# Kernel optimization log

Measured on AMD Instinct MI355X. Metric: run time of the kernel, lower is better.

Reference implementation:

```python
import jax, jax.numpy as jnp
import numpy as np

NUM_USERS = 100000
NUM_ITEMS = 200000
EMB_DIM = 64
NUM_LAYERS = 3
NUM_INTER = 1000000
BATCH = 16384


def setup_inputs() -> dict:
    key = jax.random.key(0)
    k1, k2, k3, k4, k5, k6, k7 = jax.random.split(key, 7)
    # xavier-uniform-ish init for embeddings
    bound_u = float(np.sqrt(6.0 / (NUM_USERS + EMB_DIM)))
    bound_i = float(np.sqrt(6.0 / (NUM_ITEMS + EMB_DIM)))
    user_emb = jax.random.uniform(k1, (NUM_USERS, EMB_DIM), jnp.float32, -bound_u, bound_u)
    item_emb = jax.random.uniform(k2, (NUM_ITEMS, EMB_DIM), jnp.float32, -bound_i, bound_i)
    layer_weights = jax.random.uniform(k3, (NUM_LAYERS + 1,), jnp.float32)
    inter_users = jax.random.randint(k4, (NUM_INTER,), 0, NUM_USERS, jnp.int32)
    inter_items = jax.random.randint(k5, (NUM_INTER,), 0, NUM_ITEMS, jnp.int32)
    user_ids = jax.random.randint(k6, (BATCH,), 0, NUM_USERS, jnp.int32)
    item_ids = jax.random.randint(k7, (BATCH,), 0, NUM_ITEMS, jnp.int32)
    return {
        "user_emb": user_emb,
        "item_emb": item_emb,
        "layer_weights": layer_weights,
        "inter_users": inter_users,
        "inter_items": inter_items,
        "user_ids": user_ids,
        "item_ids": item_ids,
    }


def reference(user_emb, item_emb, layer_weights, inter_users, inter_items, user_ids, item_ids):
    n_users = user_emb.shape[0]
    n_items = item_emb.shape[0]
    n_nodes = n_users + n_items

    # Symmetrized bipartite edge list: (u -> i+n_users) and (i+n_users -> u)
    rows = inter_users
    cols = inter_items + n_users
    src = jnp.concatenate([rows, cols])  # [2E]
    dst = jnp.concatenate([cols, rows])  # [2E]

    # Symmetric degree normalization: D^{-1/2} A D^{-1/2}
    deg = jax.ops.segment_sum(jnp.ones_like(src, dtype=jnp.float32), src,
                              num_segments=n_nodes)
    dinv = jnp.where(deg > 0, jax.lax.rsqrt(jnp.maximum(deg, 1.0)) * (deg > 0), 0.0)
    dinv = jnp.where(deg > 0, deg ** -0.5, 0.0)
    edge_w = dinv[src] * dinv[dst]  # [2E]

    emb = jnp.concatenate([user_emb, item_emb], axis=0)  # [N, D]
    weights = jax.nn.softmax(layer_weights)

    final = weights[0] * emb
    for layer in range(NUM_LAYERS):
        # SpMM: out[src] += w * emb[dst]
        emb = jax.ops.segment_sum(edge_w[:, None] * emb[dst], src,
                                  num_segments=n_nodes)
        final = final + weights[layer + 1] * emb

    u_final = final[:n_users]
    i_final = final[n_users:]

    user_vectors = u_final[user_ids]   # [B, D]
    item_vectors = i_final[item_ids]   # [B, D]
    scores = jnp.sum(user_vectors * item_vectors, axis=1)  # [B]
    return scores
```

## Files before the change

kernel.cpp:

```cpp
#include <hip/hip_runtime.h>
#include <math.h>

#define NUM_USERS 100000
#define NUM_ITEMS 200000
#define N_NODES   300000
#define EMB       64
#define NUM_INTER 1000000
#define N_EDGES   (2 * NUM_INTER)
#define MAX_SLOTS (N_EDGES + 3 * N_NODES + 16)
#define BATCH     16384

#define BSHIFT 9
#define BNODES 512
#define NBKT   ((N_NODES + BNODES - 1) / BNODES)
#define CAP    6144
#define EDGES_PER_BLOCK 4096
#define AB_BLOCKS ((NUM_INTER + EDGES_PER_BLOCK - 1) / EDGES_PER_BLOCK)

#define CONV_BLOCKS ((N_NODES * 8 + 255) / 256)
#define MARK_BLOCKS ((BATCH * 2) / 256)
#define PROP_BLOCKS ((N_NODES * 8 + 255) / 256)

typedef float    vfloat4 __attribute__((ext_vector_type(4)));
typedef int      vint4   __attribute__((ext_vector_type(4)));
typedef _Float16 half8   __attribute__((ext_vector_type(8)));

__global__ __launch_bounds__(256) void bucket_scatter_k(
        const int* __restrict__ iu, const int* __restrict__ ii,
        int* __restrict__ cursor , uint2* __restrict__ pairs) {
    __shared__ int hist[NBKT];
    __shared__ int gbase[NBKT];
    int tid = threadIdx.x;
    for (int b = tid; b < NBKT; b += 256) hist[b] = 0;
    __syncthreads();

    int e0 = blockIdx.x * EDGES_PER_BLOCK;
    int u[16], it[16];
    unsigned pk[32];
    #pragma unroll
    for (int k = 0; k < 16; ++k) {
        int e = e0 + k * 256 + tid;
        bool v = (e < NUM_INTER);
        u[k]  = v ? iu[e] : -1;
        it[k] = v ? (NUM_USERS + ii[e]) : -1;
    }
    #pragma unroll
    for (int k = 0; k < 16; ++k) {
        if (u[k] >= 0) {
            int b0 = u[k] >> BSHIFT;
            int r0 = atomicAdd(&hist[b0], 1);
            pk[2 * k] = ((unsigned)b0 << 13) | (unsigned)r0;
            int b1 = it[k] >> BSHIFT;
            int r1 = atomicAdd(&hist[b1], 1);
            pk[2 * k + 1] = ((unsigned)b1 << 13) | (unsigned)r1;
        }
    }
    __syncthreads();
    for (int b = tid; b < NBKT; b += 256) {
        int c = hist[b];
        if (c) gbase[b] = atomicAdd(&cursor[b * 16], c);
    }
    __syncthreads();
    #pragma unroll
    for (int k = 0; k < 16; ++k) {
        if (u[k] >= 0) {
            unsigned p0 = pk[2 * k];
            int b0 = (int)(p0 >> 13);
            int s0 = gbase[b0] + (int)(p0 & 0x1fffu);
            if (s0 < CAP) pairs[(size_t)b0 * CAP + s0] = make_uint2((unsigned)u[k], (unsigned)it[k]);
            unsigned p1 = pk[2 * k + 1];
            int b1 = (int)(p1 >> 13);
            int s1 = gbase[b1] + (int)(p1 & 0x1fffu);
            if (s1 < CAP) pairs[(size_t)b1 * CAP + s1] = make_uint2((unsigned)it[k], (unsigned)u[k]);
        }
    }
}

__global__ __launch_bounds__(256) void bucket_deg_k(
        const int* __restrict__ cursor, const uint2* __restrict__ pairs,
        int* __restrict__ deg, float* __restrict__ dinv, float* __restrict__ d2,
        float* __restrict__ rcp, int* __restrict__ lofs, int* __restrict__ bkt_padded) {
    __shared__ int cnt[BNODES];
    __shared__ int sc[256];
    int b = blockIdx.x, tid = threadIdx.x;
    cnt[tid] = 0; cnt[tid + 256] = 0;
    __syncthreads();
    int n = cursor[b * 16]; if (n > CAP) n = CAP;
    const uint2* p = pairs + (size_t)b * CAP;
    for (int j = tid; j < n; j += 256)
        atomicAdd(&cnt[p[j].x & (BNODES - 1)], 1);
    __syncthreads();

    int l0 = 2 * tid, l1 = 2 * tid + 1;
    int c0 = cnt[l0], c1 = cnt[l1];
    int p0 = (c0 + 3) & ~3, p1 = (c1 + 3) & ~3;
    int s = p0 + p1;
    sc[tid] = s;
    __syncthreads();
    for (int o = 1; o < 256; o <<= 1) {
        int x = (tid >= o) ? sc[tid - o] : 0;
        __syncthreads();
        sc[tid] += x;
        __syncthreads();
    }
    int excl = sc[tid] - s;
    int g0 = (b << BSHIFT) + l0;
    int g1 = g0 + 1;
    if (g0 < N_NODES) {
        deg[g0] = c0;
        float fd = (float)c0;
        dinv[g0] = (c0 > 0) ? (1.0f / sqrtf(fd)) : 0.0f;
        d2[g0]   = (c0 > 0) ? (1.0f / fd) : 0.0f;
        rcp[g0]  = (c0 > 0) ? sqrtf(fd) : 0.0f;
        lofs[g0] = excl;
    }
    if (g1 < N_NODES) {
        deg[g1] = c1;
        float fd = (float)c1;
        dinv[g1] = (c1 > 0) ? (1.0f / sqrtf(fd)) : 0.0f;
        d2[g1]   = (c1 > 0) ? (1.0f / fd) : 0.0f;
        rcp[g1]  = (c1 > 0) ? sqrtf(fd) : 0.0f;
        lofs[g1] = excl + p0;
    }
    if (tid == 255) bkt_padded[b] = sc[255];
}

__global__ void csr_mid_k(const int* __restrict__ bkt_padded, int* __restrict__ bkt_base,
                          int* __restrict__ row_start,
                          const float* __restrict__ lw, float* __restrict__ w,
                          _Float16* __restrict__ semb, _Float16* __restrict__ z1,
                          _Float16* __restrict__ z2) {
    __shared__ int lds[1024];
    int t = threadIdx.x;
    int v = (t < NBKT) ? bkt_padded[t] : 0;
    lds[t] = v;
    __syncthreads();
    for (int o = 1; o < 1024; o <<= 1) {
        int x = (t >= o) ? lds[t - o] : 0;
        __syncthreads();
        lds[t] += x;
        __syncthreads();
    }
    if (t < NBKT) bkt_base[t] = lds[t] - v;
    if (t == 1023) row_start[N_NODES] = lds[1023];
    if (t < 96) {
        unsigned* p = (t < 32) ? (unsigned*)semb : (t < 64) ? (unsigned*)z1 : (unsigned*)z2;
        p[(size_t)N_NODES * 32 + (t & 31)] = 0u;
    }
    if (t == 0) {
        float a = lw[0], b = lw[1], c = lw[2], d = lw[3];
        float m = fmaxf(fmaxf(a, b), fmaxf(c, d));
        float e0 = expf(a - m), e1 = expf(b - m), e2 = expf(c - m), e3 = expf(d - m);
        float sm = e0 + e1 + e2 + e3;
        w[0] = e0 / sm; w[1] = e1 / sm; w[2] = e2 / sm; w[3] = e3 / sm;
    }
}

__global__ __launch_bounds__(256) void bucket_build_k(
        const int* __restrict__ cursor, const uint2* __restrict__ pairs,
        const int* __restrict__ bkt_base, const int* __restrict__ lofs,
        int* __restrict__ row_start, int* __restrict__ nbr,
        const float* __restrict__ dinv,
        const float* __restrict__ ue, const float* __restrict__ ie,
        _Float16* __restrict__ semb) {
    int bid = blockIdx.x;
    int tid = threadIdx.x;
    if (bid >= NBKT) {
        int t = (bid - NBKT) * 256 + tid;
        int node = t >> 3;
        int q = t & 7;
        if (node >= N_NODES) return;
        const float4* src = (node < NUM_USERS)
            ? (const float4*)ue + (size_t)node * 16
            : (const float4*)ie + (size_t)(node - NUM_USERS) * 16;
        float4 f0 = src[q * 2];
        float4 f1 = src[q * 2 + 1];
        float s = dinv[node];
        half8 h;
        h[0] = (_Float16)(s * f0.x); h[1] = (_Float16)(s * f0.y);
        h[2] = (_Float16)(s * f0.z); h[3] = (_Float16)(s * f0.w);
        h[4] = (_Float16)(s * f1.x); h[5] = (_Float16)(s * f1.y);
        h[6] = (_Float16)(s * f1.z); h[7] = (_Float16)(s * f1.w);
        ((half8*)semb)[(size_t)node * 8 + q] = h;
        return;
    }
    __shared__ int ofs[BNODES];
    __shared__ int cnt2[BNODES];
    int b = bid;
    int base = bkt_base[b];
    {
        int g0 = (b << BSHIFT) + tid;
        int g1 = g0 + 256;
        int o0 = (g0 < N_NODES) ? lofs[g0] : 0;
        int o1 = (g1 < N_NODES) ? lofs[g1] : 0;
        ofs[tid] = o0; ofs[tid + 256] = o1;
        cnt2[tid] = 0; cnt2[tid + 256] = 0;
        if (g0 < N_NODES) row_start[g0] = base + o0;
        if (g1 < N_NODES) row_start[g1] = base + o1;
    }
    __syncthreads();
    int n = cursor[b * 16]; if (n > CAP) n = CAP;
    const uint2* p = pairs + (size_t)b * CAP;
    for (int j = tid; j < n; j += 256) {
        uint2 pr = p[j];
        int l = (int)(pr.x & (BNODES - 1));
        int r = atomicAdd(&cnt2[l], 1);
        nbr[base + ofs[l] + r] = (int)pr.y;
    }
}

__global__ void mark_prop_k(const int* __restrict__ row_start, const int* __restrict__ nbr,
                            const int* __restrict__ deg, const float* __restrict__ d2,
                            const _Float16* __restrict__ semb, _Float16* __restrict__ z1,
                            const int* __restrict__ uid, const int* __restrict__ iid,
                            int* __restrict__ flag) {
    int bid = blockIdx.x;
    if (bid < MARK_BLOCKS) {
        int t = bid * 256 + threadIdx.x;
        int slot = t >> 1;
        int node = (t & 1) ? (NUM_USERS + iid[slot]) : uid[slot];
        flag[node] = 1;
        int beg = row_start[node];
        int lim = beg + deg[node];
        for (int j = beg; j < lim; ++j) flag[nbr[j]] = 1;
        return;
    }
    int t = (bid - MARK_BLOCKS) * 256 + threadIdx.x;
    int node = t >> 3;
    int q = t & 7;
    if (node >= N_NODES) return;
    int beg = row_start[node], end = row_start[node + 1];
    int lim = beg + deg[node];
    const half8* src = (const half8*)semb;
    float a0 = 0.f, a1 = 0.f, a2 = 0.f, a3 = 0.f, a4 = 0.f, a5 = 0.f, a6 = 0.f, a7 = 0.f;
    for (int j = beg; j < end; j += 8) {
        vint4 na = __builtin_nontemporal_load((const vint4*)(nbr + j));
        vint4 nb = __builtin_nontemporal_load((const vint4*)(nbr + j + 4));
        #pragma unroll
        for (int k = 0; k < 8; ++k) {
            int id = (j + k < lim) ? ((k < 4) ? na[k] : nb[k - 4]) : N_NODES;
            half8 h = src[(size_t)id * 8 + q];
            a0 += (float)h[0]; a1 += (float)h[1]; a2 += (float)h[2]; a3 += (float)h[3];
            a4 += (float)h[4]; a5 += (float)h[5]; a6 += (float)h[6]; a7 += (float)h[7];
        }
    }
    float s = d2[node];
    half8 r;
    r[0] = (_Float16)(s * a0); r[1] = (_Float16)(s * a1);
    r[2] = (_Float16)(s * a2); r[3] = (_Float16)(s * a3);
    r[4] = (_Float16)(s * a4); r[5] = (_Float16)(s * a5);
    r[6] = (_Float16)(s * a6); r[7] = (_Float16)(s * a7);
    __builtin_nontemporal_store(r, (half8*)z1 + (size_t)node * 8 + q);
}

__global__ void prop_masked_k(const int* __restrict__ row_start, const int* __restrict__ nbr,
                              const int* __restrict__ deg, const float* __restrict__ d2,
                              const int* __restrict__ flag,
                              const _Float16* __restrict__ in, _Float16* __restrict__ out) {
    int t = blockIdx.x * blockDim.x + threadIdx.x;
    int node = t >> 3;
    int q = t & 7;
    if (node >= N_NODES) return;
    if (!flag[node]) return;
    int beg = row_start[node], end = row_start[node + 1];
    int lim = beg + deg[node];
    const half8* src = (const half8*)in;
    float a0 = 0.f, a1 = 0.f, a2 = 0.f, a3 = 0.f, a4 = 0.f, a5 = 0.f, a6 = 0.f, a7 = 0.f;
    for (int j = beg; j < end; j += 8) {
        vint4 na = __builtin_nontemporal_load((const vint4*)(nbr + j));
        vint4 nb = __builtin_nontemporal_load((const vint4*)(nbr + j + 4));
        #pragma unroll
        for (int k = 0; k < 8; ++k) {
            int id = (j + k < lim) ? ((k < 4) ? na[k] : nb[k - 4]) : N_NODES;
            half8 h = src[(size_t)id * 8 + q];
            a0 += (float)h[0]; a1 += (float)h[1]; a2 += (float)h[2]; a3 += (float)h[3];
            a4 += (float)h[4]; a5 += (float)h[5]; a6 += (float)h[6]; a7 += (float)h[7];
        }
    }
    float s = d2[node];
    half8 r;
    r[0] = (_Float16)(s * a0); r[1] = (_Float16)(s * a1);
    r[2] = (_Float16)(s * a2); r[3] = (_Float16)(s * a3);
    r[4] = (_Float16)(s * a4); r[5] = (_Float16)(s * a5);
    r[6] = (_Float16)(s * a6); r[7] = (_Float16)(s * a7);
    __builtin_nontemporal_store(r, (half8*)out + (size_t)node * 8 + q);
}

__global__ void fused_score_k(const int* __restrict__ row_start, const int* __restrict__ nbr,
                              const int* __restrict__ deg,
                              const float* __restrict__ dinv, const float* __restrict__ rcp,
                              const float* __restrict__ ue, const float* __restrict__ ie,
                              const _Float16* __restrict__ z1, const _Float16* __restrict__ z2,
                              const int* __restrict__ uid, const int* __restrict__ iid,
                              const float* __restrict__ w4, float* __restrict__ out) {
    int t = blockIdx.x * blockDim.x + threadIdx.x;
    int slot = t >> 4;
    if (slot >= BATCH) return;
    int within = t & 15;
    int side = within >> 3;
    int q = within & 7;

    int node;
    const float4* erow;
    if (side == 0) {
        int u = uid[slot];
        node = u;
        erow = (const float4*)ue + (size_t)u * 16;
    } else {
        int ii_ = iid[slot];
        node = NUM_USERS + ii_;
        erow = (const float4*)ie + (size_t)ii_ * 16;
    }

    float w0 = w4[0], w1 = w4[1], w2 = w4[2], w3 = w4[3];
    int beg = row_start[node], end = row_start[node + 1];
    int lim = beg + deg[node];
    const half8* z2v = (const half8*)z2;

    float a0 = 0.f, a1 = 0.f, a2 = 0.f, a3 = 0.f, a4 = 0.f, a5 = 0.f, a6 = 0.f, a7 = 0.f;
    for (int j = beg; j < end; j += 8) {
        vint4 na = __builtin_nontemporal_load((const vint4*)(nbr + j));
        vint4 nb = __builtin_nontemporal_load((const vint4*)(nbr + j + 4));
        #pragma unroll
        for (int k = 0; k < 8; ++k) {
            int id = (j + k < lim) ? ((k < 4) ? na[k] : nb[k - 4]) : N_NODES;
            half8 h = z2v[(size_t)id * 8 + q];
            a0 += (float)h[0]; a1 += (float)h[1]; a2 += (float)h[2]; a3 += (float)h[3];
            a4 += (float)h[4]; a5 += (float)h[5]; a6 += (float)h[6]; a7 += (float)h[7];
        }
    }

    float r  = rcp[node];
    float di = dinv[node];
    float e[8];
    *reinterpret_cast<float4*>(&e[0]) = erow[q * 2];
    *reinterpret_cast<float4*>(&e[4]) = erow[q * 2 + 1];
    half8 h1 = ((const half8*)z1)[(size_t)node * 8 + q];
    half8 h2 = z2v[(size_t)node * 8 + q];
    float acc[8] = {a0, a1, a2, a3, a4, a5, a6, a7};

    float f[8];
    #pragma unroll
    for (int d = 0; d < 8; ++d)
        f[d] = w0 * e[d] + r * (w1 * (float)h1[d] + w2 * (float)h2[d]) + w3 * di * acc[d];

    float p = 0.f;
    #pragma unroll
    for (int d = 0; d < 8; ++d) {
        float o = __shfl_xor(f[d], 8);
        p += f[d] * o;
    }
    p += __shfl_xor(p, 1);
    p += __shfl_xor(p, 2);
    p += __shfl_xor(p, 4);

    if (within == 0) out[slot] = p;
}


extern "C" void kernel_launch(void* const* d_in, const int* in_sizes, int n_in,
                              void* d_out, int out_size, void* d_ws, size_t ws_size,
                              hipStream_t stream) {
    const float* user_emb = (const float*)d_in[0];
    const float* item_emb = (const float*)d_in[1];
    const float* layer_w  = (const float*)d_in[2];
    const int*   inter_u  = (const int*)d_in[3];
    const int*   inter_i  = (const int*)d_in[4];
    const int*   user_ids = (const int*)d_in[5];
    const int*   item_ids = (const int*)d_in[6];
    float* out = (float*)d_out;

    char* base = (char*)d_ws;
    size_t off = 0;
    auto alloc = [&](size_t bytes) -> char* {
        char* p = base + off;
        off = (off + bytes + 255) & ~(size_t)255;
        return p;
    };
    float*    w4        = (float*)    alloc(4 * sizeof(float));
    int*      deg       = (int*)      alloc((size_t)N_NODES * sizeof(int));
    float*    dinv      = (float*)    alloc((size_t)N_NODES * sizeof(float));
    float*    d2        = (float*)    alloc((size_t)N_NODES * sizeof(float));
    float*    rcp       = (float*)    alloc((size_t)N_NODES * sizeof(float));
    int*      lofs      = (int*)      alloc((size_t)N_NODES * sizeof(int));
    int*      row_start = (int*)      alloc(((size_t)N_NODES + 1) * sizeof(int));
    int*      bkt_pad   = (int*)      alloc((size_t)NBKT * sizeof(int));
    int*      bkt_base  = (int*)      alloc((size_t)NBKT * sizeof(int));
    int*      flag      = (int*)      alloc((size_t)N_NODES * sizeof(int));
    int*      cursor    = (int*)      alloc((size_t)NBKT * 16 * sizeof(int));
    uint2*    pairs     = (uint2*)    alloc((size_t)NBKT * CAP * sizeof(uint2));
    int*      csr_nbr   = (int*)      alloc((size_t)MAX_SLOTS * sizeof(int));
    _Float16* semb      = (_Float16*) alloc(((size_t)N_NODES + 1) * EMB * sizeof(_Float16));
    _Float16* zA        = (_Float16*) alloc(((size_t)N_NODES + 1) * EMB * sizeof(_Float16));
    _Float16* zB        = (_Float16*) alloc(((size_t)N_NODES + 1) * EMB * sizeof(_Float16));

    size_t span = (size_t)((char*)cursor - (char*)flag) + (size_t)NBKT * 16 * sizeof(int);
    hipMemsetAsync(flag, 0, span, stream);

    bucket_scatter_k<<<AB_BLOCKS, 256, 0, stream>>>(inter_u, inter_i, cursor, pairs);

    bucket_deg_k<<<NBKT, 256, 0, stream>>>(cursor, pairs, deg, dinv, d2, rcp, lofs, bkt_pad);

    csr_mid_k<<<1, 1024, 0, stream>>>(bkt_pad, bkt_base, row_start, layer_w, w4, semb, zB, zA);

    bucket_build_k<<<NBKT + CONV_BLOCKS, 256, 0, stream>>>(
        cursor, pairs, bkt_base, lofs, row_start, csr_nbr, dinv, user_emb, item_emb, semb);

    mark_prop_k<<<MARK_BLOCKS + PROP_BLOCKS, 256, 0, stream>>>(
        row_start, csr_nbr, deg, d2, semb, zB, user_ids, item_ids, flag);

    prop_masked_k<<<PROP_BLOCKS, 256, 0, stream>>>(
        row_start, csr_nbr, deg, d2, flag, zB, zA);

    fused_score_k<<<(BATCH * 16 + 255) / 256, 256, 0, stream>>>(
        row_start, csr_nbr, deg, dinv, rcp, user_emb, item_emb,
        zB , zA , user_ids, item_ids, w4, out);
}
```

Baseline: 280.4 us.

## Fuse all stages into one cooperative persistent kernel with grid syncs

Replaces the memset and seven separate kernel launches with a single cooperative mega-kernel. Stages are separated by grid.sync, and the embedding conversion uses an atomic work counter for dynamic scheduling. Query-node neighbour marking moves into the degree pass through a byte qflag array, and scattering now runs two passes over contiguous edge ranges. The aim is to remove launch gaps and tail effects between kernels, at the cost of grid-wide barrier overhead and a grid capped by occupancy.

```diff
diff --git a/kernel.cpp b/kernel.cpp
--- a/kernel.cpp
+++ b/kernel.cpp
@@ -1,375 +1,364 @@
 #include <hip/hip_runtime.h>
+#include <hip/hip_cooperative_groups.h>
 #include <math.h>
+
+namespace cg = cooperative_groups;
 
 #define NUM_USERS 100000
 #define NUM_ITEMS 200000
 #define N_NODES   300000
 #define EMB       64
 #define NUM_INTER 1000000
-#define N_EDGES   (2 * NUM_INTER)
-#define MAX_SLOTS (N_EDGES + 3 * N_NODES + 16)
+#define MAX_SLOTS (2 * NUM_INTER + 3 * N_NODES + 16)
 #define BATCH     16384
 
 #define BSHIFT 9
 #define BNODES 512
 #define NBKT   ((N_NODES + BNODES - 1) / BNODES)
 #define CAP    6144
-#define EDGES_PER_BLOCK 4096
-#define AB_BLOCKS ((NUM_INTER + EDGES_PER_BLOCK - 1) / EDGES_PER_BLOCK)
-
-#define CONV_BLOCKS ((N_NODES * 8 + 255) / 256)
-#define MARK_BLOCKS ((BATCH * 2) / 256)
-#define PROP_BLOCKS ((N_NODES * 8 + 255) / 256)
-
-typedef float    vfloat4 __attribute__((ext_vector_type(4)));
-typedef int      vint4   __attribute__((ext_vector_type(4)));
-typedef _Float16 half8   __attribute__((ext_vector_type(8)));
-
-__global__ __launch_bounds__(256) void bucket_scatter_k(
-        const int* __restrict__ iu, const int* __restrict__ ii,
-        int* __restrict__ cursor , uint2* __restrict__ pairs) {
-    __shared__ int hist[NBKT];
-    __shared__ int gbase[NBKT];
-    int tid = threadIdx.x;
-    for (int b = tid; b < NBKT; b += 256) hist[b] = 0;
-    __syncthreads();
-
-    int e0 = blockIdx.x * EDGES_PER_BLOCK;
-    int u[16], it[16];
-    unsigned pk[32];
-    #pragma unroll
-    for (int k = 0; k < 16; ++k) {
-        int e = e0 + k * 256 + tid;
-        bool v = (e < NUM_INTER);
-        u[k]  = v ? iu[e] : -1;
-        it[k] = v ? (NUM_USERS + ii[e]) : -1;
-    }
-    #pragma unroll
-    for (int k = 0; k < 16; ++k) {
-        if (u[k] >= 0) {
-            int b0 = u[k] >> BSHIFT;
-            int r0 = atomicAdd(&hist[b0], 1);
-            pk[2 * k] = ((unsigned)b0 << 13) | (unsigned)r0;
-            int b1 = it[k] >> BSHIFT;
-            int r1 = atomicAdd(&hist[b1], 1);
-            pk[2 * k + 1] = ((unsigned)b1 << 13) | (unsigned)r1;
-        }
-    }
-    __syncthreads();
-    for (int b = tid; b < NBKT; b += 256) {
-        int c = hist[b];
-        if (c) gbase[b] = atomicAdd(&cursor[b * 16], c);
-    }
-    __syncthreads();
-    #pragma unroll
-    for (int k = 0; k < 16; ++k) {
-        if (u[k] >= 0) {
-            unsigned p0 = pk[2 * k];
-            int b0 = (int)(p0 >> 13);
-            int s0 = gbase[b0] + (int)(p0 & 0x1fffu);
-            if (s0 < CAP) pairs[(size_t)b0 * CAP + s0] = make_uint2((unsigned)u[k], (unsigned)it[k]);
-            unsigned p1 = pk[2 * k + 1];
-            int b1 = (int)(p1 >> 13);
-            int s1 = gbase[b1] + (int)(p1 & 0x1fffu);
-            if (s1 < CAP) pairs[(size_t)b1 * CAP + s1] = make_uint2((unsigned)it[k], (unsigned)u[k]);
-        }
-    }
-}
-
-__global__ __launch_bounds__(256) void bucket_deg_k(
-        const int* __restrict__ cursor, const uint2* __restrict__ pairs,
-        int* __restrict__ deg, float* __restrict__ dinv, float* __restrict__ d2,
-        float* __restrict__ rcp, int* __restrict__ lofs, int* __restrict__ bkt_padded) {
-    __shared__ int cnt[BNODES];
-    __shared__ int sc[256];
-    int b = blockIdx.x, tid = threadIdx.x;
-    cnt[tid] = 0; cnt[tid + 256] = 0;
-    __syncthreads();
-    int n = cursor[b * 16]; if (n > CAP) n = CAP;
-    const uint2* p = pairs + (size_t)b * CAP;
-    for (int j = tid; j < n; j += 256)
-        atomicAdd(&cnt[p[j].x & (BNODES - 1)], 1);
-    __syncthreads();
-
-    int l0 = 2 * tid, l1 = 2 * tid + 1;
-    int c0 = cnt[l0], c1 = cnt[l1];
-    int p0 = (c0 + 3) & ~3, p1 = (c1 + 3) & ~3;
-    int s = p0 + p1;
-    sc[tid] = s;
-    __syncthreads();
-    for (int o = 1; o < 256; o <<= 1) {
-        int x = (tid >= o) ? sc[tid - o] : 0;
-        __syncthreads();
-        sc[tid] += x;
-        __syncthreads();
-    }
-    int excl = sc[tid] - s;
-    int g0 = (b << BSHIFT) + l0;
-    int g1 = g0 + 1;
-    if (g0 < N_NODES) {
-        deg[g0] = c0;
-        float fd = (float)c0;
-        dinv[g0] = (c0 > 0) ? (1.0f / sqrtf(fd)) : 0.0f;
-        d2[g0]   = (c0 > 0) ? (1.0f / fd) : 0.0f;
-        rcp[g0]  = (c0 > 0) ? sqrtf(fd) : 0.0f;
-        lofs[g0] = excl;
-    }
-    if (g1 < N_NODES) {
-        deg[g1] = c1;
-        float fd = (float)c1;
-        dinv[g1] = (c1 > 0) ? (1.0f / sqrtf(fd)) : 0.0f;
-        d2[g1]   = (c1 > 0) ? (1.0f / fd) : 0.0f;
-        rcp[g1]  = (c1 > 0) ? sqrtf(fd) : 0.0f;
-        lofs[g1] = excl + p0;
-    }
-    if (tid == 255) bkt_padded[b] = sc[255];
-}
-
-__global__ void csr_mid_k(const int* __restrict__ bkt_padded, int* __restrict__ bkt_base,
-                          int* __restrict__ row_start,
-                          const float* __restrict__ lw, float* __restrict__ w,
-                          _Float16* __restrict__ semb, _Float16* __restrict__ z1,
-                          _Float16* __restrict__ z2) {
-    __shared__ int lds[1024];
-    int t = threadIdx.x;
-    int v = (t < NBKT) ? bkt_padded[t] : 0;
-    lds[t] = v;
-    __syncthreads();
-    for (int o = 1; o < 1024; o <<= 1) {
-        int x = (t >= o) ? lds[t - o] : 0;
-        __syncthreads();
-        lds[t] += x;
-        __syncthreads();
-    }
-    if (t < NBKT) bkt_base[t] = lds[t] - v;
-    if (t == 1023) row_start[N_NODES] = lds[1023];
-    if (t < 96) {
-        unsigned* p = (t < 32) ? (unsigned*)semb : (t < 64) ? (unsigned*)z1 : (unsigned*)z2;
-        p[(size_t)N_NODES * 32 + (t & 31)] = 0u;
-    }
-    if (t == 0) {
-        float a = lw[0], b = lw[1], c = lw[2], d = lw[3];
-        float m = fmaxf(fmaxf(a, b), fmaxf(c, d));
-        float e0 = expf(a - m), e1 = expf(b - m), e2 = expf(c - m), e3 = expf(d - m);
-        float sm = e0 + e1 + e2 + e3;
-        w[0] = e0 / sm; w[1] = e1 / sm; w[2] = e2 / sm; w[3] = e3 / sm;
-    }
-}
-
-__global__ __launch_bounds__(256) void bucket_build_k(
-        const int* __restrict__ cursor, const uint2* __restrict__ pairs,
-        const int* __restrict__ bkt_base, const int* __restrict__ lofs,
-        int* __restrict__ row_start, int* __restrict__ nbr,
-        const float* __restrict__ dinv,
-        const float* __restrict__ ue, const float* __restrict__ ie,
-        _Float16* __restrict__ semb) {
-    int bid = blockIdx.x;
-    int tid = threadIdx.x;
-    if (bid >= NBKT) {
-        int t = (bid - NBKT) * 256 + tid;
+#define NSCAT  490
+#define CONV_UNITS ((N_NODES * 8) / 256)
+
+typedef int      vint4 __attribute__((ext_vector_type(4)));
+typedef _Float16 half8 __attribute__((ext_vector_type(8)));
+
+struct Params {
+    const float* ue; const float* ie; const float* lw;
+    const int* iu; const int* ii; const int* uid; const int* iid;
+    float* out;
+    int* cursor; uint2* pairs;
+    int* deg; float* dinv; float* d2; float* rcp;
+    int* lofs; int* row_start; int* bkt_pad; int* bkt_base;
+    int* flag; unsigned char* qflag; int* work;
+    int* nbr;
+    _Float16* semb; _Float16* z1; _Float16* z2;
+    float* w4;
+};
+
+__global__ __launch_bounds__(256) void mega_k(Params P) {
+    cg::grid_group grid = cg::this_grid();
+    const int tid  = threadIdx.x;
+    const int bid  = blockIdx.x;
+    const int nblk = gridDim.x;
+    const int gt   = nblk * 256;
+    const int g    = bid * 256 + tid;
+
+    __shared__ int smem[1184];
+    __shared__ int wsh;
+
+    for (int i = g; i < N_NODES; i += gt) P.flag[i] = 0;
+    unsigned* q4 = (unsigned*)P.qflag;
+    for (int i = g; i < (N_NODES + 3) / 4; i += gt) q4[i] = 0u;
+    for (int i = g; i < NBKT * 16; i += gt) P.cursor[i] = 0;
+    if (g == 0) P.work[0] = 0;
+    grid.sync();
+
+    {
+        int qb = nblk < 16 ? nblk : 16;
+        if (bid < qb) {
+            for (int k = bid * 256 + tid; k < BATCH * 2; k += qb * 256) {
+                int node = (k & 1) ? (NUM_USERS + P.iid[k >> 1]) : P.uid[k >> 1];
+                P.qflag[node] = 1;
+                P.flag[node]  = 1;
+            }
+        }
+        int nscat = nblk < NSCAT ? nblk : NSCAT;
+        if (bid < nscat) {
+            int* hist = smem;
+            int* gb   = smem + NBKT;
+            for (int b = tid; b < NBKT; b += 256) hist[b] = 0;
+            __syncthreads();
+            int per = (NUM_INTER + nscat - 1) / nscat;
+            int e0 = bid * per;
+            int e1 = (e0 + per < NUM_INTER) ? e0 + per : NUM_INTER;
+            for (int e = e0 + tid; e < e1; e += 256) {
+                int u  = P.iu[e];
+                int it = NUM_USERS + P.ii[e];
+                atomicAdd(&hist[u >> BSHIFT], 1);
+                atomicAdd(&hist[it >> BSHIFT], 1);
+            }
+            __syncthreads();
+            for (int b = tid; b < NBKT; b += 256) {
+                int c = hist[b];
+                gb[b] = c ? atomicAdd(&P.cursor[b * 16], c) : 0;
+                hist[b] = 0;
+            }
+            __syncthreads();
+            for (int e = e0 + tid; e < e1; e += 256) {
+                int u  = P.iu[e];
+                int it = NUM_USERS + P.ii[e];
+                int b0 = u >> BSHIFT;
+                int r0 = atomicAdd(&hist[b0], 1);
+                int s0 = gb[b0] + r0;
+                if (s0 < CAP) P.pairs[(size_t)b0 * CAP + s0] = make_uint2((unsigned)u, (unsigned)it);
+                int b1 = it >> BSHIFT;
+                int r1 = atomicAdd(&hist[b1], 1);
+                int s1 = gb[b1] + r1;
+                if (s1 < CAP) P.pairs[(size_t)b1 * CAP + s1] = make_uint2((unsigned)it, (unsigned)u);
+            }
+        }
+    }
+    grid.sync();
+
+    for (int b = bid; b < NBKT; b += nblk) {
+        int* cnt = smem;
+        int* sc  = smem + BNODES;
+        cnt[tid] = 0; cnt[tid + 256] = 0;
+        __syncthreads();
+        int n = P.cursor[b * 16]; if (n > CAP) n = CAP;
+        const uint2* p = P.pairs + (size_t)b * CAP;
+        for (int j = tid; j < n; j += 256) {
+            uint2 pr = p[j];
+            atomicAdd(&cnt[(int)pr.x & (BNODES - 1)], 1);
+            if (P.qflag[pr.x]) P.flag[pr.y] = 1;
+        }
+        __syncthreads();
+        int l0 = 2 * tid, l1 = 2 * tid + 1;
+        int c0 = cnt[l0], c1 = cnt[l1];
+        int p0 = (c0 + 3) & ~3, p1 = (c1 + 3) & ~3;
+        int s = p0 + p1;
+        sc[tid] = s;
+        __syncthreads();
+        for (int o = 1; o < 256; o <<= 1) {
+            int x = (tid >= o) ? sc[tid - o] : 0;
+            __syncthreads();
+            sc[tid] += x;
+            __syncthreads();
+        }
+        int excl = sc[tid] - s;
+        int g0 = (b << BSHIFT) + l0;
+        int g1 = g0 + 1;
+        if (g0 < N_NODES) {
+            P.deg[g0] = c0;
+            float fd = (float)c0;
+            P.dinv[g0] = (c0 > 0) ? (1.0f / sqrtf(fd)) : 0.0f;
+            P.d2[g0]   = (c0 > 0) ? (1.0f / fd) : 0.0f;
+            P.rcp[g0]  = (c0 > 0) ? sqrtf(fd) : 0.0f;
+            P.lofs[g0] = excl;
+        }
+        if (g1 < N_NODES) {
+            P.deg[g1] = c1;
+            float fd = (float)c1;
+            P.dinv[g1] = (c1 > 0) ? (1.0f / sqrtf(fd)) : 0.0f;
+            P.d2[g1]   = (c1 > 0) ? (1.0f / fd) : 0.0f;
+            P.rcp[g1]  = (c1 > 0) ? sqrtf(fd) : 0.0f;
+            P.lofs[g1] = excl + p0;
+        }
+        if (tid == 255) P.bkt_pad[b] = sc[255];
+        __syncthreads();
+    }
+    grid.sync();
+
+    if (bid == 0) {
+        int i0 = 3 * tid;
+        int v0 = (i0     < NBKT) ? P.bkt_pad[i0]     : 0;
+        int v1 = (i0 + 1 < NBKT) ? P.bkt_pad[i0 + 1] : 0;
+        int v2 = (i0 + 2 < NBKT) ? P.bkt_pad[i0 + 2] : 0;
+        int s = v0 + v1 + v2;
+        int* sc = smem;
+        sc[tid] = s;
+        __syncthreads();
+        for (int o = 1; o < 256; o <<= 1) {
+            int x = (tid >= o) ? sc[tid - o] : 0;
+            __syncthreads();
+            sc[tid] += x;
+            __syncthreads();
+        }
+        int excl = sc[tid] - s;
+        if (i0     < NBKT) P.bkt_base[i0]     = excl;
+        if (i0 + 1 < NBKT) P.bkt_base[i0 + 1] = excl + v0;
+        if (i0 + 2 < NBKT) P.bkt_base[i0 + 2] = excl + v0 + v1;
+        if (tid == 255) P.row_start[N_NODES] = sc[255];
+        if (tid < 96) {
+            unsigned* pz = (tid < 32) ? (unsigned*)P.semb
+                         : (tid < 64) ? (unsigned*)P.z1 : (unsigned*)P.z2;
+            pz[(size_t)N_NODES * 32 + (tid & 31)] = 0u;
+        }
+        if (tid == 0) {
+            float a = P.lw[0], b = P.lw[1], c = P.lw[2], d = P.lw[3];
+            float m = fmaxf(fmaxf(a, b), fmaxf(c, d));
+            float e0 = expf(a - m), e1 = expf(b - m), e2 = expf(c - m), e3 = expf(d - m);
+            float sm = e0 + e1 + e2 + e3;
+            P.w4[0] = e0 / sm; P.w4[1] = e1 / sm; P.w4[2] = e2 / sm; P.w4[3] = e3 / sm;
+        }
+    }
+    grid.sync();
+
+    for (int b = bid; b < NBKT; b += nblk) {
+        int* ofs  = smem;
+        int* cnt2 = smem + BNODES;
+        int base = P.bkt_base[b];
+        int g0 = (b << BSHIFT) + tid;
+        int g1 = g0 + 256;
+        int o0 = (g0 < N_NODES) ? P.lofs[g0] : 0;
+        int o1 = (g1 < N_NODES) ? P.lofs[g1] : 0;
+        ofs[tid] = o0; ofs[tid + 256] = o1;
+        cnt2[tid] = 0; cnt2[tid + 256] = 0;
+        if (g0 < N_NODES) P.row_start[g0] = base + o0;
+        if (g1 < N_NODES) P.row_start[g1] = base + o1;
+        __syncthreads();
+        int n = P.cursor[b * 16]; if (n > CAP) n = CAP;
+        const uint2* p = P.pairs + (size_t)b * CAP;
+        for (int j = tid; j < n; j += 256) {
+            uint2 pr = p[j];
+            int l = (int)pr.x & (BNODES - 1);
+            int r = atomicAdd(&cnt2[l], 1);
+            P.nbr[base + ofs[l] + r] = (int)pr.y;
+        }
+        __syncthreads();
+    }
+    while (true) {
+        if (tid == 0) wsh = atomicAdd(P.work, 1);
+        __syncthreads();
+        int w = wsh;
+        __syncthreads();
+        if (w >= CONV_UNITS) break;
+        int t = w * 256 + tid;
         int node = t >> 3;
         int q = t & 7;
-        if (node >= N_NODES) return;
         const float4* src = (node < NUM_USERS)
-            ? (const float4*)ue + (size_t)node * 16
-            : (const float4*)ie + (size_t)(node - NUM_USERS) * 16;
+            ? (const float4*)P.ue + (size_t)node * 16
+            : (const float4*)P.ie + (size_t)(node - NUM_USERS) * 16;
         float4 f0 = src[q * 2];
         float4 f1 = src[q * 2 + 1];
-        float s = dinv[node];
+        float sdi = P.dinv[node];
         half8 h;
-        h[0] = (_Float16)(s * f0.x); h[1] = (_Float16)(s * f0.y);
-        h[2] = (_Float16)(s * f0.z); h[3] = (_Float16)(s * f0.w);
-        h[4] = (_Float16)(s * f1.x); h[5] = (_Float16)(s * f1.y);
-        h[6] = (_Float16)(s * f1.z); h[7] = (_Float16)(s * f1.w);
-        ((half8*)semb)[(size_t)node * 8 + q] = h;
-        return;
-    }
-    __shared__ int ofs[BNODES];
-    __shared__ int cnt2[BNODES];
-    int b = bid;
-    int base = bkt_base[b];
-    {
-        int g0 = (b << BSHIFT) + tid;
-        int g1 = g0 + 256;
-        int o0 = (g0 < N_NODES) ? lofs[g0] : 0;
-        int o1 = (g1 < N_NODES) ? lofs[g1] : 0;
-        ofs[tid] = o0; ofs[tid + 256] = o1;
-        cnt2[tid] = 0; cnt2[tid + 256] = 0;
-        if (g0 < N_NODES) row_start[g0] = base + o0;
-        if (g1 < N_NODES) row_start[g1] = base + o1;
-    }
-    __syncthreads();
-    int n = cursor[b * 16]; if (n > CAP) n = CAP;
-    const uint2* p = pairs + (size_t)b * CAP;
-    for (int j = tid; j < n; j += 256) {
-        uint2 pr = p[j];
-        int l = (int)(pr.x & (BNODES - 1));
-        int r = atomicAdd(&cnt2[l], 1);
-        nbr[base + ofs[l] + r] = (int)pr.y;
-    }
-}
-
-__global__ void mark_prop_k(const int* __restrict__ row_start, const int* __restrict__ nbr,
-                            const int* __restrict__ deg, const float* __restrict__ d2,
-                            const _Float16* __restrict__ semb, _Float16* __restrict__ z1,
-                            const int* __restrict__ uid, const int* __restrict__ iid,
-                            int* __restrict__ flag) {
-    int bid = blockIdx.x;
-    if (bid < MARK_BLOCKS) {
-        int t = bid * 256 + threadIdx.x;
-        int slot = t >> 1;
-        int node = (t & 1) ? (NUM_USERS + iid[slot]) : uid[slot];
-        flag[node] = 1;
-        int beg = row_start[node];
-        int lim = beg + deg[node];
-        for (int j = beg; j < lim; ++j) flag[nbr[j]] = 1;
-        return;
-    }
-    int t = (bid - MARK_BLOCKS) * 256 + threadIdx.x;
-    int node = t >> 3;
-    int q = t & 7;
-    if (node >= N_NODES) return;
-    int beg = row_start[node], end = row_start[node + 1];
-    int lim = beg + deg[node];
-    const half8* src = (const half8*)semb;
-    float a0 = 0.f, a1 = 0.f, a2 = 0.f, a3 = 0.f, a4 = 0.f, a5 = 0.f, a6 = 0.f, a7 = 0.f;
-    for (int j = beg; j < end; j += 8) {
-        vint4 na = __builtin_nontemporal_load((const vint4*)(nbr + j));
-        vint4 nb = __builtin_nontemporal_load((const vint4*)(nbr + j + 4));
+        h[0] = (_Float16)(sdi * f0.x); h[1] = (_Float16)(sdi * f0.y);
+        h[2] = (_Float16)(sdi * f0.z); h[3] = (_Float16)(sdi * f0.w);
+        h[4] = (_Float16)(sdi * f1.x); h[5] = (_Float16)(sdi * f1.y);
+        h[6] = (_Float16)(sdi * f1.z); h[7] = (_Float16)(sdi * f1.w);
+        ((half8*)P.semb)[(size_t)node * 8 + q] = h;
+    }
+    grid.sync();
+
+    for (int v0 = bid * 32; v0 < N_NODES; v0 += nblk * 32) {
+        int node = v0 + (tid >> 3);
+        int q = tid & 7;
+        if (node < N_NODES) {
+            int beg = P.row_start[node], end = P.row_start[node + 1];
+            int lim = beg + P.deg[node];
+            const half8* src = (const half8*)P.semb;
+            float a0=0.f,a1=0.f,a2=0.f,a3=0.f,a4=0.f,a5=0.f,a6=0.f,a7=0.f;
+            for (int j = beg; j < end; j += 8) {
+                vint4 na  = __builtin_nontemporal_load((const vint4*)(P.nbr + j));
+                vint4 nb4 = __builtin_nontemporal_load((const vint4*)(P.nbr + j + 4));
+                #pragma unroll
+                for (int k = 0; k < 8; ++k) {
+                    int id = (j + k < lim) ? ((k < 4) ? na[k] : nb4[k - 4]) : N_NODES;
+                    half8 h = src[(size_t)id * 8 + q];
+                    a0 += (float)h[0]; a1 += (float)h[1]; a2 += (float)h[2]; a3 += (float)h[3];
+                    a4 += (float)h[4]; a5 += (float)h[5]; a6 += (float)h[6]; a7 += (float)h[7];
+                }
+            }
+            float sd = P.d2[node];
+            half8 r;
+            r[0] = (_Float16)(sd * a0); r[1] = (_Float16)(sd * a1);
+            r[2] = (_Float16)(sd * a2); r[3] = (_Float16)(sd * a3);
+            r[4] = (_Float16)(sd * a4); r[5] = (_Float16)(sd * a5);
+            r[6] = (_Float16)(sd * a6); r[7] = (_Float16)(sd * a7);
+            __builtin_nontemporal_store(r, (half8*)P.z1 + (size_t)node * 8 + q);
+        }
+    }
+    grid.sync();
+
+    for (int v0 = bid * 32; v0 < N_NODES; v0 += nblk * 32) {
+        int node = v0 + (tid >> 3);
+        int q = tid & 7;
+        if (node < N_NODES && P.flag[node]) {
+            int beg = P.row_start[node], end = P.row_start[node + 1];
+            int lim = beg + P.deg[node];
+            const half8* src = (const half8*)P.z1;
+            float a0=0.f,a1=0.f,a2=0.f,a3=0.f,a4=0.f,a5=0.f,a6=0.f,a7=0.f;
+            for (int j = beg; j < end; j += 8) {
+                vint4 na  = __builtin_nontemporal_load((const vint4*)(P.nbr + j));
+                vint4 nb4 = __builtin_nontemporal_load((const vint4*)(P.nbr + j + 4));
+                #pragma unroll
+                for (int k = 0; k < 8; ++k) {
+                    int id = (j + k < lim) ? ((k < 4) ? na[k] : nb4[k - 4]) : N_NODES;
+                    half8 h = src[(size_t)id * 8 + q];
+                    a0 += (float)h[0]; a1 += (float)h[1]; a2 += (float)h[2]; a3 += (float)h[3];
+                    a4 += (float)h[4]; a5 += (float)h[5]; a6 += (float)h[6]; a7 += (float)h[7];
+                }
+            }
+            float sd = P.d2[node];
+            half8 r;
+            r[0] = (_Float16)(sd * a0); r[1] = (_Float16)(sd * a1);
+            r[2] = (_Float16)(sd * a2); r[3] = (_Float16)(sd * a3);
+            r[4] = (_Float16)(sd * a4); r[5] = (_Float16)(sd * a5);
+            r[6] = (_Float16)(sd * a6); r[7] = (_Float16)(sd * a7);
+            __builtin_nontemporal_store(r, (half8*)P.z2 + (size_t)node * 8 + q);
+        }
+    }
+    grid.sync();
+
+    for (int s0 = g; s0 < BATCH * 16; s0 += gt) {
+        int slot = s0 >> 4;
+        int within = s0 & 15;
+        int side = within >> 3;
+        int q = within & 7;
+
+        int node;
+        const float4* erow;
+        if (side == 0) {
+            int u = P.uid[slot];
+            node = u;
+            erow = (const float4*)P.ue + (size_t)u * 16;
+        } else {
+            int ii_ = P.iid[slot];
+            node = NUM_USERS + ii_;
+            erow = (const float4*)P.ie + (size_t)ii_ * 16;
+        }
+
+        float w0 = P.w4[0], w1 = P.w4[1], w2 = P.w4[2], w3 = P.w4[3];
+        int beg = P.row_start[node], end = P.row_start[node + 1];
+        int lim = beg + P.deg[node];
+        const half8* z2v = (const half8*)P.z2;
+
+        float a0=0.f,a1=0.f,a2=0.f,a3=0.f,a4=0.f,a5=0.f,a6=0.f,a7=0.f;
+        for (int j = beg; j < end; j += 8) {
+            vint4 na  = __builtin_nontemporal_load((const vint4*)(P.nbr + j));
+            vint4 nb4 = __builtin_nontemporal_load((const vint4*)(P.nbr + j + 4));
+            #pragma unroll
+            for (int k = 0; k < 8; ++k) {
+                int id = (j + k < lim) ? ((k < 4) ? na[k] : nb4[k - 4]) : N_NODES;
+                half8 h = z2v[(size_t)id * 8 + q];
+                a0 += (float)h[0]; a1 += (float)h[1]; a2 += (float)h[2]; a3 += (float)h[3];
+                a4 += (float)h[4]; a5 += (float)h[5]; a6 += (float)h[6]; a7 += (float)h[7];
+            }
+        }
+
+        float r  = P.rcp[node];
+        float di = P.dinv[node];
+        float e[8];
+        *reinterpret_cast<float4*>(&e[0]) = erow[q * 2];
+        *reinterpret_cast<float4*>(&e[4]) = erow[q * 2 + 1];
+        half8 h1 = ((const half8*)P.z1)[(size_t)node * 8 + q];
+        half8 h2 = z2v[(size_t)node * 8 + q];
+        float acc[8] = {a0, a1, a2, a3, a4, a5, a6, a7};
+
+        float f[8];
         #pragma unroll
-        for (int k = 0; k < 8; ++k) {
-            int id = (j + k < lim) ? ((k < 4) ? na[k] : nb[k - 4]) : N_NODES;
-            half8 h = src[(size_t)id * 8 + q];
-            a0 += (float)h[0]; a1 += (float)h[1]; a2 += (float)h[2]; a3 += (float)h[3];
-            a4 += (float)h[4]; a5 += (float)h[5]; a6 += (float)h[6]; a7 += (float)h[7];
-        }
-    }
-    float s = d2[node];
-    half8 r;
-    r[0] = (_Float16)(s * a0); r[1] = (_Float16)(s * a1);
-    r[2] = (_Float16)(s * a2); r[3] = (_Float16)(s * a3);
-    r[4] = (_Float16)(s * a4); r[5] = (_Float16)(s * a5);
-    r[6] = (_Float16)(s * a6); r[7] = (_Float16)(s * a7);
-    __builtin_nontemporal_store(r, (half8*)z1 + (size_t)node * 8 + q);
-}
-
-__global__ void prop_masked_k(const int* __restrict__ row_start, const int* __restrict__ nbr,
-                              const int* __restrict__ deg, const float* __restrict__ d2,
-                              const int* __restrict__ flag,
-                              const _Float16* __restrict__ in, _Float16* __restrict__ out) {
-    int t = blockIdx.x * blockDim.x + threadIdx.x;
-    int node = t >> 3;
-    int q = t & 7;
-    if (node >= N_NODES) return;
-    if (!flag[node]) return;
-    int beg = row_start[node], end = row_start[node + 1];
-    int lim = beg + deg[node];
-    const half8* src = (const half8*)in;
-    float a0 = 0.f, a1 = 0.f, a2 = 0.f, a3 = 0.f, a4 = 0.f, a5 = 0.f, a6 = 0.f, a7 = 0.f;
-    for (int j = beg; j < end; j += 8) {
-        vint4 na = __builtin_nontemporal_load((const vint4*)(nbr + j));
-        vint4 nb = __builtin_nontemporal_load((const vint4*)(nbr + j + 4));
+        for (int d = 0; d < 8; ++d)
+            f[d] = w0 * e[d] + r * (w1 * (float)h1[d] + w2 * (float)h2[d]) + w3 * di * acc[d];
+
+        float pr = 0.f;
         #pragma unroll
-        for (int k = 0; k < 8; ++k) {
-            int id = (j + k < lim) ? ((k < 4) ? na[k] : nb[k - 4]) : N_NODES;
-            half8 h = src[(size_t)id * 8 + q];
-            a0 += (float)h[0]; a1 += (float)h[1]; a2 += (float)h[2]; a3 += (float)h[3];
-            a4 += (float)h[4]; a5 += (float)h[5]; a6 += (float)h[6]; a7 += (float)h[7];
-        }
-    }
-    float s = d2[node];
-    half8 r;
-    r[0] = (_Float16)(s * a0); r[1] = (_Float16)(s * a1);
-    r[2] = (_Float16)(s * a2); r[3] = (_Float16)(s * a3);
-    r[4] = (_Float16)(s * a4); r[5] = (_Float16)(s * a5);
-    r[6] = (_Float16)(s * a6); r[7] = (_Float16)(s * a7);
-    __builtin_nontemporal_store(r, (half8*)out + (size_t)node * 8 + q);
-}
-
-__global__ void fused_score_k(const int* __restrict__ row_start, const int* __restrict__ nbr,
-                              const int* __restrict__ deg,
-                              const float* __restrict__ dinv, const float* __restrict__ rcp,
-                              const float* __restrict__ ue, const float* __restrict__ ie,
-                              const _Float16* __restrict__ z1, const _Float16* __restrict__ z2,
-                              const int* __restrict__ uid, const int* __restrict__ iid,
-                              const float* __restrict__ w4, float* __restrict__ out) {
-    int t = blockIdx.x * blockDim.x + threadIdx.x;
-    int slot = t >> 4;
-    if (slot >= BATCH) return;
-    int within = t & 15;
-    int side = within >> 3;
-    int q = within & 7;
-
-    int node;
-    const float4* erow;
-    if (side == 0) {
-        int u = uid[slot];
-        node = u;
-        erow = (const float4*)ue + (size_t)u * 16;
-    } else {
-        int ii_ = iid[slot];
-        node = NUM_USERS + ii_;
-        erow = (const float4*)ie + (size_t)ii_ * 16;
-    }
-
-    float w0 = w4[0], w1 = w4[1], w2 = w4[2], w3 = w4[3];
-    int beg = row_start[node], end = row_start[node + 1];
-    int lim = beg + deg[node];
-    const half8* z2v = (const half8*)z2;
-
-    float a0 = 0.f, a1 = 0.f, a2 = 0.f, a3 = 0.f, a4 = 0.f, a5 = 0.f, a6 = 0.f, a7 = 0.f;
-    for (int j = beg; j < end; j += 8) {
-        vint4 na = __builtin_nontemporal_load((const vint4*)(nbr + j));
-        vint4 nb = __builtin_nontemporal_load((const vint4*)(nbr + j + 4));
-        #pragma unroll
-        for (int k = 0; k < 8; ++k) {
-            int id = (j + k < lim) ? ((k < 4) ? na[k] : nb[k - 4]) : N_NODES;
-            half8 h = z2v[(size_t)id * 8 + q];
-            a0 += (float)h[0]; a1 += (float)h[1]; a2 += (float)h[2]; a3 += (float)h[3];
-            a4 += (float)h[4]; a5 += (float)h[5]; a6 += (float)h[6]; a7 += (float)h[7];
-        }
-    }
-
-    float r  = rcp[node];
-    float di = dinv[node];
-    float e[8];
-    *reinterpret_cast<float4*>(&e[0]) = erow[q * 2];
-    *reinterpret_cast<float4*>(&e[4]) = erow[q * 2 + 1];
-    half8 h1 = ((const half8*)z1)[(size_t)node * 8 + q];
-    half8 h2 = z2v[(size_t)node * 8 + q];
-    float acc[8] = {a0, a1, a2, a3, a4, a5, a6, a7};
-
-    float f[8];
-    #pragma unroll
-    for (int d = 0; d < 8; ++d)
-        f[d] = w0 * e[d] + r * (w1 * (float)h1[d] + w2 * (float)h2[d]) + w3 * di * acc[d];
-
-    float p = 0.f;
-    #pragma unroll
-    for (int d = 0; d < 8; ++d) {
-        float o = __shfl_xor(f[d], 8);
-        p += f[d] * o;
-    }
-    p += __shfl_xor(p, 1);
-    p += __shfl_xor(p, 2);
-    p += __shfl_xor(p, 4);
-
-    if (within == 0) out[slot] = p;
+        for (int d = 0; d < 8; ++d) {
+            float o = __shfl_xor(f[d], 8);
+            pr += f[d] * o;
+        }
+        pr += __shfl_xor(pr, 1);
+        pr += __shfl_xor(pr, 2);
+        pr += __shfl_xor(pr, 4);
+
+        if (within == 0) P.out[slot] = pr;
+    }
 }
 
 
 extern "C" void kernel_launch(void* const* d_in, const int* in_sizes, int n_in,
                               void* d_out, int out_size, void* d_ws, size_t ws_size,
                               hipStream_t stream) {
-    const float* user_emb = (const float*)d_in[0];
-    const float* item_emb = (const float*)d_in[1];
-    const float* layer_w  = (const float*)d_in[2];
-    const int*   inter_u  = (const int*)d_in[3];
-    const int*   inter_i  = (const int*)d_in[4];
-    const int*   user_ids = (const int*)d_in[5];
-    const int*   item_ids = (const int*)d_in[6];
-    float* out = (float*)d_out;
-
     char* base = (char*)d_ws;
     size_t off = 0;
     auto alloc = [&](size_t bytes) -> char* {
@@ -377,42 +366,52 @@
         off = (off + bytes + 255) & ~(size_t)255;
         return p;
     };
-    float*    w4        = (float*)    alloc(4 * sizeof(float));
-    int*      deg       = (int*)      alloc((size_t)N_NODES * sizeof(int));
-    float*    dinv      = (float*)    alloc((size_t)N_NODES * sizeof(float));
-    float*    d2        = (float*)    alloc((size_t)N_NODES * sizeof(float));
-    float*    rcp       = (float*)    alloc((size_t)N_NODES * sizeof(float));
-    int*      lofs      = (int*)      alloc((size_t)N_NODES * sizeof(int));
-    int*      row_start = (int*)      alloc(((size_t)N_NODES + 1) * sizeof(int));
-    int*      bkt_pad   = (int*)      alloc((size_t)NBKT * sizeof(int));
-    int*      bkt_base  = (int*)      alloc((size_t)NBKT * sizeof(int));
-    int*      flag      = (int*)      alloc((size_t)N_NODES * sizeof(int));
-    int*      cursor    = (int*)      alloc((size_t)NBKT * 16 * sizeof(int));
-    uint2*    pairs     = (uint2*)    alloc((size_t)NBKT * CAP * sizeof(uint2));
-    int*      csr_nbr   = (int*)      alloc((size_t)MAX_SLOTS * sizeof(int));
-    _Float16* semb      = (_Float16*) alloc(((size_t)N_NODES + 1) * EMB * sizeof(_Float16));
-    _Float16* zA        = (_Float16*) alloc(((size_t)N_NODES + 1) * EMB * sizeof(_Float16));
-    _Float16* zB        = (_Float16*) alloc(((size_t)N_NODES + 1) * EMB * sizeof(_Float16));
-
-    size_t span = (size_t)((char*)cursor - (char*)flag) + (size_t)NBKT * 16 * sizeof(int);
-    hipMemsetAsync(flag, 0, span, stream);
-
-    bucket_scatter_k<<<AB_BLOCKS, 256, 0, stream>>>(inter_u, inter_i, cursor, pairs);
-
-    bucket_deg_k<<<NBKT, 256, 0, stream>>>(cursor, pairs, deg, dinv, d2, rcp, lofs, bkt_pad);
-
-    csr_mid_k<<<1, 1024, 0, stream>>>(bkt_pad, bkt_base, row_start, layer_w, w4, semb, zB, zA);
-
-    bucket_build_k<<<NBKT + CONV_BLOCKS, 256, 0, stream>>>(
-        cursor, pairs, bkt_base, lofs, row_start, csr_nbr, dinv, user_emb, item_emb, semb);
-
-    mark_prop_k<<<MARK_BLOCKS + PROP_BLOCKS, 256, 0, stream>>>(
-        row_start, csr_nbr, deg, d2, semb, zB, user_ids, item_ids, flag);
-
-    prop_masked_k<<<PROP_BLOCKS, 256, 0, stream>>>(
-        row_start, csr_nbr, deg, d2, flag, zB, zA);
-
-    fused_score_k<<<(BATCH * 16 + 255) / 256, 256, 0, stream>>>(
-        row_start, csr_nbr, deg, dinv, rcp, user_emb, item_emb,
-        zB , zA , user_ids, item_ids, w4, out);
+
+    Params P;
+    P.ue  = (const float*)d_in[0];
+    P.ie  = (const float*)d_in[1];
+    P.lw  = (const float*)d_in[2];
+    P.iu  = (const int*)d_in[3];
+    P.ii  = (const int*)d_in[4];
+    P.uid = (const int*)d_in[5];
+    P.iid = (const int*)d_in[6];
+    P.out = (float*)d_out;
+
+    P.w4        = (float*)    alloc(4 * sizeof(float));
+    P.deg       = (int*)      alloc((size_t)N_NODES * sizeof(int));
+    P.dinv      = (float*)    alloc((size_t)N_NODES * sizeof(float));
+    P.d2        = (float*)    alloc((size_t)N_NODES * sizeof(float));
+    P.rcp       = (float*)    alloc((size_t)N_NODES * sizeof(float));
+    P.lofs      = (int*)      alloc((size_t)N_NODES * sizeof(int));
+    P.row_start = (int*)      alloc(((size_t)N_NODES + 1) * sizeof(int));
+    P.bkt_pad   = (int*)      alloc((size_t)NBKT * sizeof(int));
+    P.bkt_base  = (int*)      alloc((size_t)NBKT * sizeof(int));
+    P.flag      = (int*)      alloc((size_t)N_NODES * sizeof(int));
+    P.qflag     = (unsigned char*)alloc((size_t)N_NODES + 4);
+    P.work      = (int*)      alloc(256);
+    P.cursor    = (int*)      alloc((size_t)NBKT * 16 * sizeof(int));
+    P.pairs     = (uint2*)    alloc((size_t)NBKT * CAP * sizeof(uint2));
+    P.nbr       = (int*)      alloc((size_t)MAX_SLOTS * sizeof(int));
+    P.semb      = (_Float16*) alloc(((size_t)N_NODES + 1) * EMB * sizeof(_Float16));
+    P.z1        = (_Float16*) alloc(((size_t)N_NODES + 1) * EMB * sizeof(_Float16));
+    P.z2        = (_Float16*) alloc(((size_t)N_NODES + 1) * EMB * sizeof(_Float16));
+
+    static int g_grid = 0;
+    if (g_grid == 0) {
+        int dev = 0;
+        hipGetDevice(&dev);
+        hipDeviceProp_t prop{};
+        hipGetDeviceProperties(&prop, dev);
+        int bpc = 0;
+        hipOccupancyMaxActiveBlocksPerMultiprocessor(&bpc, (const void*)mega_k, 256, 0);
+        if (bpc < 1) bpc = 1;
+        long gg = (long)bpc * (long)prop.multiProcessorCount;
+        if (gg > 2048) gg = 2048;
+        if (gg < 1) gg = 1;
+        g_grid = (int)gg;
+    }
+
+    void* args[] = { (void*)&P };
+    hipLaunchCooperativeKernel((const void*)mega_k, dim3(g_grid), dim3(256),
+                               args, 0, stream);
 }
```

Measured after the change: 841.4 us. 200% more time.
